# Optimization experiments

Hardware: AMD Instinct MI355X
Metric: run time of the kernel (lower is better)

Reference implementation:

```python
import jax, jax.numpy as jnp
import numpy as np

NUM_CLASSES = 1000
MARGIN = 1.0
COS_EPS = 1e-8   # torch F.cosine_similarity eps
NORM_EPS = 1e-12 # torch F.normalize eps


def setup_inputs() -> dict:
    key = jax.random.key(0)
    k1, k2 = jax.random.split(key)
    N, D = 65536, 256
    embeddings = jax.random.normal(k1, (N, D), dtype=jnp.float32)
    labels = jax.random.randint(k2, (N,), 0, NUM_CLASSES)
    return {"embeddings": embeddings, "labels": labels}


def reference(embeddings, labels):
    N = embeddings.shape[0]
    # L2-normalize embeddings (torch F.normalize with eps clamp on norm)
    e_norm = jnp.maximum(jnp.linalg.norm(embeddings, axis=1, keepdims=True), NORM_EPS)
    e = embeddings / e_norm  # [N, D], unit rows

    # Per-class mean of normalized embeddings; zero vector for empty classes
    sums = jax.ops.segment_sum(e, labels, num_segments=NUM_CLASSES)          # [C, D]
    counts = jax.ops.segment_sum(jnp.ones((N,), e.dtype), labels,
                                 num_segments=NUM_CLASSES)                    # [C]
    centers = sums / jnp.maximum(counts, 1.0)[:, None]                        # [C, D]

    # cosine_similarity(e_i, center_j) = (e_i . c_j) / max(||e_i||*||c_j||, eps)
    # ||e_i|| == 1 (up to the normalize clamp), so denom = max(||c_j||, eps)
    c_norm = jnp.linalg.norm(centers, axis=1)                                 # [C]
    denom = jnp.maximum(c_norm, COS_EPS)
    sims = (e @ centers.T) / denom[None, :]                                   # [N, C]

    rows = jnp.arange(N)
    pos = jnp.square(sims[rows, labels] - 1.0)                                # [N]
    neg_all = jnp.square(jax.nn.relu(MARGIN - sims))                          # [N, C]
    neg_at_label = neg_all[rows, labels]                                      # [N]
    neg = (neg_all.sum(axis=1) - neg_at_label) / (NUM_CLASSES - 1)            # [N]

    return jnp.mean(pos + neg)
```

## Files before the change

### kernel.cpp

```cpp
#include <hip/hip_runtime.h>
#include <hip/hip_bf16.h>

#define NROWS 65536
#define DIM   256
#define NCLS  1000
#define CPAD  1024

typedef __attribute__((ext_vector_type(8))) short bf16x8;
typedef __attribute__((ext_vector_type(4))) float f32x4;

__device__ inline unsigned short f2bf(float x) {
    unsigned int u = __builtin_bit_cast(unsigned int, x);
    unsigned int lsb = (u >> 16) & 1u;
    u += 0x7fffu + lsb;
    return (unsigned short)(u >> 16);
}

__device__ inline float bf2f(unsigned short u) {
    unsigned int v = ((unsigned int)u) << 16;
    return __builtin_bit_cast(float, v);
}

__device__ inline void gload_lds16(const void* g, void* l) {
    __builtin_amdgcn_global_load_lds(
        (const __attribute__((address_space(1))) unsigned int*)g,
        (__attribute__((address_space(3))) unsigned int*)l, 16, 0, 0);
}

__global__ __launch_bounds__(256) void k_norm_acc(
    const float* __restrict__ emb, const int* __restrict__ labels,
    unsigned short* __restrict__ e, unsigned int* __restrict__ counts)
{
    int gid  = blockIdx.x * 256 + threadIdx.x;
    int row  = gid >> 6;
    int lane = gid & 63;
    float4 v = ((const float4*)(emb + (size_t)row * DIM))[lane];
    float ss = v.x*v.x + v.y*v.y + v.z*v.z + v.w*v.w;
    #pragma unroll
    for (int off = 1; off < 64; off <<= 1) ss += __shfl_xor(ss, off);
    float inv = 1.0f / fmaxf(sqrtf(ss), 1e-12f);
    v.x *= inv; v.y *= inv; v.z *= inv; v.w *= inv;
    ushort4 u;
    u.x = f2bf(v.x); u.y = f2bf(v.y); u.z = f2bf(v.z); u.w = f2bf(v.w);
    ((ushort4*)(e + (size_t)row * DIM))[lane] = u;
    if (lane == 0) atomicAdd(counts + labels[row], 1u);
}

__global__ __launch_bounds__(1024) void k_prefix(
    const unsigned int* __restrict__ counts, unsigned int* __restrict__ offs,
    unsigned int* __restrict__ cursor)
{
    __shared__ unsigned int s[1024];
    int t = threadIdx.x;
    s[t] = (t < NCLS) ? counts[t] : 0u;
    __syncthreads();
    for (int d = 1; d < 1024; d <<= 1) {
        unsigned int v = (t >= d) ? s[t - d] : 0u;
        __syncthreads();
        s[t] += v;
        __syncthreads();
    }
    if (t < NCLS) {
        unsigned int excl = (t == 0) ? 0u : s[t - 1];
        offs[t]   = excl;
        cursor[t] = excl;
    }
}

__global__ __launch_bounds__(256) void k_scatter(
    const int* __restrict__ labels, unsigned int* __restrict__ cursor,
    int* __restrict__ sidx)
{
    int r = blockIdx.x * 256 + threadIdx.x;
    unsigned int pos = atomicAdd(&cursor[labels[r]], 1u);
    sidx[pos] = r;
}

__global__ __launch_bounds__(256) void k_gather_sum(
    const unsigned short* __restrict__ e, const int* __restrict__ sidx,
    const unsigned int* __restrict__ offs, const unsigned int* __restrict__ counts,
    float* __restrict__ sums)
{
    __shared__ int   sidx_s[256];
    __shared__ float part[16][256];
    const int tid = threadIdx.x;
    const int c   = blockIdx.x;
    const int rs  = tid >> 4;
    const int jc  = tid & 15;
    unsigned int beg = offs[c], cnt = counts[c];

    float a[16];
    #pragma unroll
    for (int k = 0; k < 16; ++k) a[k] = 0.0f;

    for (unsigned int base = 0; base < cnt; base += 256) {
        int m = (int)(cnt - base > 256u ? 256u : cnt - base);
        __syncthreads();
        if (tid < m) sidx_s[tid] = sidx[beg + base + tid];
        __syncthreads();
        for (int u = rs; u < m; u += 16) {
            const unsigned short* p = e + (size_t)sidx_s[u] * DIM + jc * 16;
            uint4 lo = *(const uint4*)p;
            uint4 hi = *(const uint4*)(p + 8);
            unsigned int w[8] = {lo.x, lo.y, lo.z, lo.w, hi.x, hi.y, hi.z, hi.w};
            #pragma unroll
            for (int kk = 0; kk < 8; ++kk) {
                a[2*kk]   += bf2f((unsigned short)(w[kk] & 0xffffu));
                a[2*kk+1] += bf2f((unsigned short)(w[kk] >> 16));
            }
        }
    }
    #pragma unroll
    for (int k = 0; k < 16; ++k) part[rs][jc * 16 + k] = a[k];
    __syncthreads();
    float s = 0.0f;
    #pragma unroll
    for (int r2 = 0; r2 < 16; ++r2) s += part[r2][tid];
    sums[(size_t)c * DIM + tid] = s;
}

__global__ __launch_bounds__(256) void k_centers(
    const float* __restrict__ sums, const unsigned int* __restrict__ counts,
    unsigned short* __restrict__ cs)
{
    int gid  = blockIdx.x * 256 + threadIdx.x;
    int c    = gid >> 6;
    int lane = gid & 63;
    float4 v = make_float4(0.f, 0.f, 0.f, 0.f);
    if (c < NCLS) {
        v = ((const float4*)(sums + (size_t)c * DIM))[lane];
        float ic = 1.0f / fmaxf((float)counts[c], 1.0f);
        v.x *= ic; v.y *= ic; v.z *= ic; v.w *= ic;
        float ss = v.x*v.x + v.y*v.y + v.z*v.z + v.w*v.w;
        #pragma unroll
        for (int off = 1; off < 64; off <<= 1) ss += __shfl_xor(ss, off);
        float sc = 1.0f / fmaxf(sqrtf(ss), 1e-8f);
        v.x *= sc; v.y *= sc; v.z *= sc; v.w *= sc;
    }
    ushort4 u;
    u.x = f2bf(v.x); u.y = f2bf(v.y); u.z = f2bf(v.z); u.w = f2bf(v.w);
    ((ushort4*)(cs + (size_t)c * DIM))[lane] = u;
}

#define TMB 128
#define TCB 128

__global__ __launch_bounds__(256, 2) void k_loss_mfma(
    const unsigned short* __restrict__ e, const unsigned short* __restrict__ cs,
    const int* __restrict__ labels, float* __restrict__ acc)
{
    __shared__ __align__(16) unsigned short b_s[2][TCB * 64];
    __shared__ float negsum_s[2][TMB];
    __shared__ float slab_s[TMB];
    __shared__ int   lab_s[TMB];
    __shared__ float red_s[4];

    const int tid  = threadIdx.x;
    const int row0 = blockIdx.x * TMB;
    const int wave = tid >> 6, lane = tid & 63;
    const int wm = wave >> 1, wn = wave & 1;
    const int l16 = lane & 15, q = lane >> 4;
    const int st_r = lane >> 3;
    const int st_s = (lane & 7) ^ st_r;

    if (tid < TMB) {
        lab_s[tid]  = labels[row0 + tid];
        slab_s[tid] = 0.0f;
    }

    bf16x8 af[4][4][2];
    #pragma unroll
    for (int mi = 0; mi < 4; ++mi) {
        const unsigned short* pa =
            e + (size_t)(row0 + wm*64 + mi*16 + l16) * DIM + q * 8;
        #pragma unroll
        for (int kc = 0; kc < 4; ++kc)
            #pragma unroll
            for (int kk = 0; kk < 2; ++kk)
                af[mi][kc][kk] = *(const bf16x8*)(pa + kc*64 + kk*32);
    }

    auto stageB = [&](int cb_, int kc_, int buf_) {
        #pragma unroll
        for (int ch = 0; ch < 4; ++ch) {
            int chunk = wave * 4 + ch;
            int row   = chunk * 8 + st_r;
            gload_lds16(&cs[(size_t)(cb_ * TCB + row) * DIM + kc_ * 64 + st_s * 8],
                        &b_s[buf_][chunk * 512]);
        }
    };

    float negp[4][4];
    #pragma unroll
    for (int mi = 0; mi < 4; ++mi)
        #pragma unroll
        for (int rg = 0; rg < 4; ++rg) negp[mi][rg] = 0.0f;

    stageB(0, 0, 0);

    for (int cb = 0; cb < CPAD / TCB; ++cb) {
        f32x4 accf[4][4] = {};
        #pragma unroll
        for (int kc = 0; kc < 4; ++kc) {
            int t = cb * 4 + kc;
            __syncthreads();
            if (t < 31) stageB((t + 1) >> 2, (t + 1) & 3, (t + 1) & 1);
            const unsigned short* bs = b_s[t & 1];
            #pragma unroll
            for (int kk = 0; kk < 2; ++kk) {
                bf16x8 bfr[4];
                #pragma unroll
                for (int ni = 0; ni < 4; ++ni) {
                    int rowB = wn*64 + ni*16 + l16;
                    bfr[ni] = *(const bf16x8*)&bs[rowB*64 + (((kk*4 + q) ^ (rowB & 7)) * 8)];
                }
                #pragma unroll
                for (int mi = 0; mi < 4; ++mi)
                    #pragma unroll
                    for (int ni = 0; ni < 4; ++ni)
                        accf[mi][ni] = __builtin_amdgcn_mfma_f32_16x16x32_bf16(
                            af[mi][kc][kk], bfr[ni], accf[mi][ni], 0, 0, 0);
            }
        }
        #pragma unroll
        for (int mi = 0; mi < 4; ++mi) {
            #pragma unroll
            for (int rg = 0; rg < 4; ++rg) {
                int rloc = wm*64 + mi*16 + q*4 + rg;
                int lab  = lab_s[rloc];
                #pragma unroll
                for (int ni = 0; ni < 4; ++ni) {
                    int c   = cb * TCB + wn*64 + ni*16 + l16;
                    float s = accf[mi][ni][rg];
                    if (c < NCLS) {
                        float t2 = fmaxf(1.0f - s, 0.0f);
                        negp[mi][rg] += t2 * t2;
                        if (c == lab) slab_s[rloc] = s;
                    }
                }
            }
        }
    }

    #pragma unroll
    for (int mi = 0; mi < 4; ++mi) {
        #pragma unroll
        for (int rg = 0; rg < 4; ++rg) {
            float v = negp[mi][rg];
            #pragma unroll
            for (int off = 8; off >= 1; off >>= 1) v += __shfl_down(v, off, 16);
            if (l16 == 0) negsum_s[wn][wm*64 + mi*16 + q*4 + rg] = v;
        }
    }
    __syncthreads();

    float part = 0.0f;
    if (tid < TMB) {
        float ns = negsum_s[0][tid] + negsum_s[1][tid];
        float sl = slab_s[tid];
        float t  = fmaxf(1.0f - sl, 0.0f);
        part = (sl - 1.0f) * (sl - 1.0f) + (ns - t * t) * (1.0f / 999.0f);
    }
    #pragma unroll
    for (int off = 32; off >= 1; off >>= 1) part += __shfl_down(part, off, 64);
    if (lane == 0) red_s[wave] = part;
    __syncthreads();
    if (tid == 0) atomicAdd(acc, red_s[0] + red_s[1] + red_s[2] + red_s[3]);
}

__global__ void k_final(const float* __restrict__ acc, float* __restrict__ out)
{
    if (threadIdx.x == 0) out[0] = acc[0] * (1.0f / (float)NROWS);
}

extern "C" void kernel_launch(void* const* d_in, const int* in_sizes, int n_in,
                              void* d_out, int out_size, void* d_ws, size_t ws_size,
                              hipStream_t stream)
{
    const float* emb    = (const float*)d_in[0];
    const int*   labels = (const int*)d_in[1];
    float*       out    = (float*)d_out;
    char*        ws     = (char*)d_ws;

    const size_t OFF_SUMS = (size_t)NROWS * DIM * 2;
    const size_t OFF_CNT  = OFF_SUMS + (size_t)NCLS * DIM * 4;
    const size_t OFF_ACC  = OFF_CNT + 4096;
    const size_t OFF_OFFS = OFF_ACC + 16;
    const size_t OFF_CUR  = OFF_OFFS + 4096;
    const size_t OFF_SIDX = OFF_CUR + 4096;
    const size_t OFF_CS   = OFF_SIDX + (size_t)NROWS * 4;

    unsigned short* e      = (unsigned short*)ws;
    float*          sums   = (float*)(ws + OFF_SUMS);
    unsigned int*   counts = (unsigned int*)(ws + OFF_CNT);
    float*          acc    = (float*)(ws + OFF_ACC);
    unsigned int*   offs   = (unsigned int*)(ws + OFF_OFFS);
    unsigned int*   cursor = (unsigned int*)(ws + OFF_CUR);
    int*            sidx   = (int*)(ws + OFF_SIDX);
    unsigned short* cs     = (unsigned short*)(ws + OFF_CS);

    hipMemsetAsync(ws + OFF_CNT, 0, 4096 + 16, stream);

    k_norm_acc  <<<NROWS / 4, 256, 0, stream>>>(emb, labels, e, counts);
    k_prefix    <<<1, 1024, 0, stream>>>(counts, offs, cursor);
    k_scatter   <<<NROWS / 256, 256, 0, stream>>>(labels, cursor, sidx);
    k_gather_sum<<<NCLS, 256, 0, stream>>>(e, sidx, offs, counts, sums);
    k_centers   <<<CPAD / 4, 256, 0, stream>>>(sums, counts, cs);
    k_loss_mfma <<<NROWS / TMB, 256, 0, stream>>>(e, cs, labels, acc);
    k_final     <<<1, 64, 0, stream>>>(acc, out);
}
```

Baseline: 195.6 us.

## Stage A tile in LDS, stream centers from global into registers, per-thread loss accumulation

The loss GEMM kernel now stages the whole 128x256 embedding tile into swizzled LDS once and streams center fragments straight from global memory into double-buffered registers. This removes the per-k-step __syncthreads and the LDS staging of centers. Loss terms are folded into one per-thread scalar, so the label lookup, shared slab and negsum arrays and the two-level row reduction go away. The gather-sum kernel also switches to wave-per-row coalesced ushort4 loads with a smaller partial buffer. Risks: center reads now depend on L2/global latency without LDS reuse across waves, and the larger A buffer in LDS may lower occupancy.

```diff
diff --git a/kernel.cpp b/kernel.cpp
--- a/kernel.cpp
+++ b/kernel.cpp
@@ -82,41 +82,27 @@
     float* __restrict__ sums)
 {
     __shared__ int   sidx_s[256];
-    __shared__ float part[16][256];
-    const int tid = threadIdx.x;
-    const int c   = blockIdx.x;
-    const int rs  = tid >> 4;
-    const int jc  = tid & 15;
+    __shared__ float part[4][256];
+    const int tid  = threadIdx.x;
+    const int wave = tid >> 6, lane = tid & 63;
+    const int c    = blockIdx.x;
     unsigned int beg = offs[c], cnt = counts[c];
 
-    float a[16];
-    #pragma unroll
-    for (int k = 0; k < 16; ++k) a[k] = 0.0f;
-
+    float a0 = 0.f, a1 = 0.f, a2 = 0.f, a3 = 0.f;
     for (unsigned int base = 0; base < cnt; base += 256) {
         int m = (int)(cnt - base > 256u ? 256u : cnt - base);
         __syncthreads();
         if (tid < m) sidx_s[tid] = sidx[beg + base + tid];
         __syncthreads();
-        for (int u = rs; u < m; u += 16) {
-            const unsigned short* p = e + (size_t)sidx_s[u] * DIM + jc * 16;
-            uint4 lo = *(const uint4*)p;
-            uint4 hi = *(const uint4*)(p + 8);
-            unsigned int w[8] = {lo.x, lo.y, lo.z, lo.w, hi.x, hi.y, hi.z, hi.w};
-            #pragma unroll
-            for (int kk = 0; kk < 8; ++kk) {
-                a[2*kk]   += bf2f((unsigned short)(w[kk] & 0xffffu));
-                a[2*kk+1] += bf2f((unsigned short)(w[kk] >> 16));
-            }
-        }
-    }
-    #pragma unroll
-    for (int k = 0; k < 16; ++k) part[rs][jc * 16 + k] = a[k];
-    __syncthreads();
-    float s = 0.0f;
-    #pragma unroll
-    for (int r2 = 0; r2 < 16; ++r2) s += part[r2][tid];
-    sums[(size_t)c * DIM + tid] = s;
+        for (int u = wave; u < m; u += 4) {
+            ushort4 v = ((const ushort4*)(e + (size_t)sidx_s[u] * DIM))[lane];
+            a0 += bf2f(v.x); a1 += bf2f(v.y); a2 += bf2f(v.z); a3 += bf2f(v.w);
+        }
+    }
+    ((float4*)part[wave])[lane] = make_float4(a0, a1, a2, a3);
+    __syncthreads();
+    sums[(size_t)c * DIM + tid] =
+        part[0][tid] + part[1][tid] + part[2][tid] + part[3][tid];
 }
 
 __global__ __launch_bounds__(256) void k_centers(
@@ -149,11 +135,7 @@
     const unsigned short* __restrict__ e, const unsigned short* __restrict__ cs,
     const int* __restrict__ labels, float* __restrict__ acc)
 {
-    __shared__ __align__(16) unsigned short b_s[2][TCB * 64];
-    __shared__ float negsum_s[2][TMB];
-    __shared__ float slab_s[TMB];
-    __shared__ int   lab_s[TMB];
-    __shared__ float red_s[4];
+    __shared__ __align__(16) unsigned short a_s[4][TMB * 64];
 
     const int tid  = threadIdx.x;
     const int row0 = blockIdx.x * TMB;
@@ -163,109 +145,98 @@
     const int st_r = lane >> 3;
     const int st_s = (lane & 7) ^ st_r;
 
-    if (tid < TMB) {
-        lab_s[tid]  = labels[row0 + tid];
-        slab_s[tid] = 0.0f;
-    }
-
-    bf16x8 af[4][4][2];
-    #pragma unroll
-    for (int mi = 0; mi < 4; ++mi) {
-        const unsigned short* pa =
-            e + (size_t)(row0 + wm*64 + mi*16 + l16) * DIM + q * 8;
-        #pragma unroll
-        for (int kc = 0; kc < 4; ++kc)
-            #pragma unroll
-            for (int kk = 0; kk < 2; ++kk)
-                af[mi][kc][kk] = *(const bf16x8*)(pa + kc*64 + kk*32);
-    }
-
-    auto stageB = [&](int cb_, int kc_, int buf_) {
+    int labv[16];
+    #pragma unroll
+    for (int mi = 0; mi < 4; ++mi)
+        #pragma unroll
+        for (int rg = 0; rg < 4; ++rg)
+            labv[mi * 4 + rg] = labels[row0 + wm*64 + mi*16 + q*4 + rg];
+
+    #pragma unroll
+    for (int kc = 0; kc < 4; ++kc)
         #pragma unroll
         for (int ch = 0; ch < 4; ++ch) {
             int chunk = wave * 4 + ch;
             int row   = chunk * 8 + st_r;
-            gload_lds16(&cs[(size_t)(cb_ * TCB + row) * DIM + kc_ * 64 + st_s * 8],
-                        &b_s[buf_][chunk * 512]);
-        }
-    };
-
-    float negp[4][4];
-    #pragma unroll
-    for (int mi = 0; mi < 4; ++mi)
-        #pragma unroll
-        for (int rg = 0; rg < 4; ++rg) negp[mi][rg] = 0.0f;
-
-    stageB(0, 0, 0);
+            gload_lds16(&e[(size_t)(row0 + row) * DIM + kc * 64 + st_s * 8],
+                        &a_s[kc][chunk * 512]);
+        }
+    __syncthreads();
+
+    #define LOADB(buf, cb_, kc_)                                               \
+        {                                                                      \
+            _Pragma("unroll")                                                  \
+            for (int ni = 0; ni < 4; ++ni)                                     \
+                _Pragma("unroll")                                              \
+                for (int kk = 0; kk < 2; ++kk)                                 \
+                    buf[ni][kk] = *(const bf16x8*)&cs[                         \
+                        (size_t)((cb_) * TCB + wn*64 + ni*16 + l16) * DIM      \
+                        + (kc_) * 64 + kk * 32 + q * 8];                       \
+        }
+
+    bf16x8 b0[4][2], b1[4][2];
+    LOADB(b0, 0, 0);
+
+    float la = 0.0f;
+    const float KN = 1.0f / 999.0f;
 
     for (int cb = 0; cb < CPAD / TCB; ++cb) {
         f32x4 accf[4][4] = {};
         #pragma unroll
         for (int kc = 0; kc < 4; ++kc) {
-            int t = cb * 4 + kc;
-            __syncthreads();
-            if (t < 31) stageB((t + 1) >> 2, (t + 1) & 3, (t + 1) & 1);
-            const unsigned short* bs = b_s[t & 1];
+            int ns = cb * 4 + kc + 1;
+            if (kc & 1) {
+                if (ns < 32) LOADB(b0, ns >> 2, ns & 3);
+            } else {
+                if (ns < 32) LOADB(b1, ns >> 2, ns & 3);
+            }
             #pragma unroll
             for (int kk = 0; kk < 2; ++kk) {
-                bf16x8 bfr[4];
+                bf16x8 af[4];
                 #pragma unroll
-                for (int ni = 0; ni < 4; ++ni) {
-                    int rowB = wn*64 + ni*16 + l16;
-                    bfr[ni] = *(const bf16x8*)&bs[rowB*64 + (((kk*4 + q) ^ (rowB & 7)) * 8)];
+                for (int mi = 0; mi < 4; ++mi) {
+                    int rowA = wm*64 + mi*16 + l16;
+                    af[mi] = *(const bf16x8*)&a_s[kc][
+                        rowA*64 + (((kk*4 + q) ^ (rowA & 7)) * 8)];
                 }
                 #pragma unroll
                 for (int mi = 0; mi < 4; ++mi)
                     #pragma unroll
                     for (int ni = 0; ni < 4; ++ni)
                         accf[mi][ni] = __builtin_amdgcn_mfma_f32_16x16x32_bf16(
-                            af[mi][kc][kk], bfr[ni], accf[mi][ni], 0, 0, 0);
+                            af[mi],
+                            (kc & 1) ? b1[ni][kk] : b0[ni][kk],
+                            accf[mi][ni], 0, 0, 0);
             }
         }
         #pragma unroll
         for (int mi = 0; mi < 4; ++mi) {
             #pragma unroll
             for (int rg = 0; rg < 4; ++rg) {
-                int rloc = wm*64 + mi*16 + q*4 + rg;
-                int lab  = lab_s[rloc];
+                int lab = labv[mi * 4 + rg];
                 #pragma unroll
                 for (int ni = 0; ni < 4; ++ni) {
                     int c   = cb * TCB + wn*64 + ni*16 + l16;
                     float s = accf[mi][ni][rg];
                     if (c < NCLS) {
-                        float t2 = fmaxf(1.0f - s, 0.0f);
-                        negp[mi][rg] += t2 * t2;
-                        if (c == lab) slab_s[rloc] = s;
+                        float t = fmaxf(1.0f - s, 0.0f);
+                        la += t * t * KN;
+                        if (c == lab)
+                            la += (s - 1.0f) * (s - 1.0f) - t * t * KN;
                     }
                 }
             }
         }
     }
 
-    #pragma unroll
-    for (int mi = 0; mi < 4; ++mi) {
-        #pragma unroll
-        for (int rg = 0; rg < 4; ++rg) {
-            float v = negp[mi][rg];
-            #pragma unroll
-            for (int off = 8; off >= 1; off >>= 1) v += __shfl_down(v, off, 16);
-            if (l16 == 0) negsum_s[wn][wm*64 + mi*16 + q*4 + rg] = v;
-        }
-    }
-    __syncthreads();
-
-    float part = 0.0f;
-    if (tid < TMB) {
-        float ns = negsum_s[0][tid] + negsum_s[1][tid];
-        float sl = slab_s[tid];
-        float t  = fmaxf(1.0f - sl, 0.0f);
-        part = (sl - 1.0f) * (sl - 1.0f) + (ns - t * t) * (1.0f / 999.0f);
-    }
-    #pragma unroll
-    for (int off = 32; off >= 1; off >>= 1) part += __shfl_down(part, off, 64);
-    if (lane == 0) red_s[wave] = part;
-    __syncthreads();
-    if (tid == 0) atomicAdd(acc, red_s[0] + red_s[1] + red_s[2] + red_s[3]);
+    __syncthreads();
+    float* red = (float*)&a_s[0][0];
+    #pragma unroll
+    for (int off = 32; off >= 1; off >>= 1) la += __shfl_xor(la, off);
+    if (lane == 0) red[wave] = la;
+    __syncthreads();
+    if (tid == 0) atomicAdd(acc, red[0] + red[1] + red[2] + red[3]);
+    #undef LOADB
 }
 
 __global__ void k_final(const float* __restrict__ acc, float* __restrict__ out)
```

New measurement: 370.9 us. 89.6% more time.
